# Kernel optimization log

Measured on AMD Instinct MI355X. Metric: run time of the kernel, lower is better.

The kernel has to match this reference:

```python
import jax, jax.numpy as jnp
import numpy as np

N = 50000      # ncount
L = 4          # number of wavelet scales
E = 1600000    # nnz per sparse wavelet matrix
C_IN = 128
C_OUT = 128


def setup_inputs() -> dict:
    key = jax.random.key(0)
    ks = jax.random.split(key, 7)
    return {
        "phi_indices": jax.random.randint(ks[0], (L, 2, E), 0, N, dtype=jnp.int32),
        "phi_values": jax.random.uniform(ks[1], (L, E), dtype=jnp.float32),
        "phi_inverse_indices": jax.random.randint(ks[2], (L, 2, E), 0, N, dtype=jnp.int32),
        "phi_inverse_values": jax.random.uniform(ks[3], (L, E), dtype=jnp.float32),
        "features": jax.random.normal(ks[4], (N, L, C_IN), dtype=jnp.float32),
        "weight_matrix": jax.random.normal(ks[5], (C_IN, C_OUT), dtype=jnp.float32) * (6.0 / (C_IN + C_OUT)) ** 0.5,
        "diagonal_weight_filter": jax.random.uniform(ks[6], (N,), dtype=jnp.float32, minval=0.9, maxval=1.1),
    }


def _spmm(idx, vals, X):
    # sparse [N,N] (COO rows=idx[0], cols=idx[1]) @ dense X [N,C]
    row, col = idx[0], idx[1]
    return jax.ops.segment_sum(vals[:, None] * X[col], row, num_segments=N)


def reference(phi_indices, phi_values, phi_inverse_indices, phi_inverse_values,
              features, weight_matrix, diagonal_weight_filter):
    # Original: (phi_i @ diag(theta) @ phi_inv_i) @ (features[:,i,:] @ W)
    # Applied right-to-left via associativity -> three streaming spmm-style ops,
    # never materializing the N x N product matrix.
    def per_scale(p_idx, p_val, pi_idx, pi_val, feat_i):
        y = feat_i @ weight_matrix                 # [N, C_OUT]
        y = _spmm(pi_idx, pi_val, y)               # phi_inverse @ y
        y = y * diagonal_weight_filter[:, None]    # diag(theta) @ y
        return _spmm(p_idx, p_val, y)              # phi @ y

    feats_lf = jnp.moveaxis(features, 1, 0)        # [L, N, C_IN]
    out = jax.vmap(per_scale)(phi_indices, phi_values,
                              phi_inverse_indices, phi_inverse_values, feats_lf)
    return jnp.moveaxis(out, 0, 1)                 # [N, L, C_OUT]
```

## Files before the change

kernel.cpp:

```cpp
#include <hip/hip_runtime.h>

#define N_NODES 50000
#define L_SCALES 4
#define E_NNZ 1600000
#define C 128
#define NL (N_NODES * L_SCALES)

#define ELL_W 64
#define OVF_CAP 8192

#define RPB 16
#define NB (N_NODES / RPB)
#define NSUB 8
#define SCAP 112
#define GROUP 4
#define BT_STRIDE 16

__global__ __launch_bounds__(256) void gemm_all(
    const float* __restrict__ feat,
    const float* __restrict__ W,
    float* __restrict__ Y)
{
    __shared__ float4 Xs4[64 * 32];

    int t = threadIdx.x;
    int l = t & 63;
    int c0 = __builtin_amdgcn_readfirstlane((t >> 6) << 5);
    size_t r0 = (size_t)blockIdx.x * 64;

    const float4* feat4 = (const float4*)(feat + r0 * C);
    for (int i = t; i < 64 * 32; i += 256) {
        int row = i >> 5, slot = i & 31;
        Xs4[(row << 5) | (slot ^ (row & 31))] = feat4[i];
    }
    __syncthreads();

    float acc[32];
    #pragma unroll
    for (int j = 0; j < 32; ++j) acc[j] = 0.f;

    int m = l & 31;
    for (int kt = 0; kt < C; kt += 8) {
        float4 xa = Xs4[(l << 5) | ((kt >> 2) ^ m)];
        float4 xb = Xs4[(l << 5) | (((kt >> 2) + 1) ^ m)];
        float x8[8];
        x8[0] = xa.x; x8[1] = xa.y; x8[2] = xa.z; x8[3] = xa.w;
        x8[4] = xb.x; x8[5] = xb.y; x8[6] = xb.z; x8[7] = xb.w;
        #pragma unroll
        for (int kk = 0; kk < 8; ++kk) {
            const float* wr = W + (size_t)(kt + kk) * C + c0;
            #pragma unroll
            for (int j = 0; j < 32; ++j)
                acc[j] = fmaf(x8[kk], wr[j], acc[j]);
        }
    }

    float* orow = Y + (r0 + l) * C + c0;
    #pragma unroll
    for (int j4 = 0; j4 < 8; ++j4)
        ((float4*)orow)[j4] = make_float4(acc[4*j4], acc[4*j4+1], acc[4*j4+2], acc[4*j4+3]);
}

__global__ __launch_bounds__(256) void partition_edges(
    const int*   __restrict__ rows,
    const int*   __restrict__ cols,
    const float* __restrict__ vals,
    uint2* __restrict__ bkt,
    int*   __restrict__ btail,
    int* __restrict__ ovf_n, int* __restrict__ ovf_row,
    int* __restrict__ ovf_col, float* __restrict__ ovf_val)
{
    int e = blockIdx.x * 256 + threadIdx.x;
    if (e >= E_NNZ) return;
    int s = blockIdx.x & (NSUB - 1);
    int r = rows[e];
    int c = cols[e];
    float v = vals[e];
    int b = r >> 4;
    int pos = atomicAdd(&btail[(s * NB + b) * BT_STRIDE], 1);
    if (pos < SCAP) {
        bkt[((size_t)s * NB + b) * SCAP + pos] =
            make_uint2((unsigned)c | ((unsigned)(r & (RPB - 1)) << 16), __float_as_uint(v));
    } else {
        int k = atomicAdd(ovf_n, 1);
        if (k < OVF_CAP) { ovf_row[k] = r; ovf_col[k] = c; ovf_val[k] = v; }
    }
}

__global__ __launch_bounds__(256) void ell_from_buckets(
    const uint2* __restrict__ bkt,
    const int*   __restrict__ btail,
    uint2* __restrict__ ell,
    int*   __restrict__ cnt,
    int* __restrict__ ovf_n, int* __restrict__ ovf_row,
    int* __restrict__ ovf_col, float* __restrict__ ovf_val)
{
    __shared__ __align__(16) uint2 ell_s[GROUP * RPB][ELL_W];
    __shared__ int lcnt[GROUP * RPB];

    int t  = threadIdx.x;
    int b0 = blockIdx.x * GROUP;
    int r0 = b0 * RPB;

    if (t < GROUP * RPB) lcnt[t] = 0;
    __syncthreads();

    for (int g = 0; g < GROUP; ++g) {
        int b = b0 + g;
        if (b >= NB) break;
        for (int s = 0; s < NSUB; ++s) {
            int n = btail[(s * NB + b) * BT_STRIDE];
            if (n > SCAP) n = SCAP;
            for (int i = t; i < n; i += 256) {
                uint2 rec = bkt[((size_t)s * NB + b) * SCAP + i];
                int lr = g * RPB + (int)(rec.x >> 16);
                int pos = atomicAdd(&lcnt[lr], 1);
                if (pos < ELL_W) {
                    ell_s[lr][pos] = make_uint2(rec.x & 0xFFFFu, rec.y);
                } else {
                    int k = atomicAdd(ovf_n, 1);
                    if (k < OVF_CAP) {
                        ovf_row[k] = r0 + lr;
                        ovf_col[k] = (int)(rec.x & 0xFFFFu);
                        ovf_val[k] = __uint_as_float(rec.y);
                    }
                }
            }
        }
    }
    __syncthreads();

    const uint4* src = (const uint4*)&ell_s[0][0];
    for (int i = t; i < GROUP * RPB * (ELL_W / 2); i += 256) {
        int row = r0 + (i >> 5);
        if (row < N_NODES)
            ((uint4*)ell)[(size_t)row * (ELL_W / 2) + (i & 31)] = src[i];
    }
    if (t < GROUP * RPB) {
        int row = r0 + t;
        if (row < N_NODES) cnt[row] = lcnt[t];
    }
}

__global__ __launch_bounds__(256) void spmm_ell(
    const uint2* __restrict__ ell,
    const int*   __restrict__ cnt,
    const int*   __restrict__ ovf_n,
    const int*   __restrict__ ovf_row,
    const int*   __restrict__ ovf_col,
    const float* __restrict__ ovf_val,
    const float* __restrict__ X,
    const float* __restrict__ row_scale,
    float*       __restrict__ out,
    int x_stride, int out_stride)
{
    int row  = (blockIdx.x * 256 + threadIdx.x) >> 6;
    int lane = threadIdx.x & 63;

    int n   = cnt[row];
    int ncl = n < ELL_W ? n : ELL_W;

    uint2 rec = make_uint2(0u, 0u);
    if (lane < ncl) rec = ell[(size_t)row * ELL_W + lane];
    int mycol = (int)rec.x;
    int myval = (int)rec.y;

    float2 acc = {0.f, 0.f};
    int j = 0;
    for (; j + 8 <= ncl; j += 8) {
        float2 x[8];
        #pragma unroll
        for (int u = 0; u < 8; ++u) {
            int c = __builtin_amdgcn_readlane(mycol, j + u);
            x[u] = ((const float2*)(X + (size_t)c * x_stride))[lane];
        }
        #pragma unroll
        for (int u = 0; u < 8; ++u) {
            float v = __uint_as_float((unsigned)__builtin_amdgcn_readlane(myval, j + u));
            acc.x = fmaf(v, x[u].x, acc.x);
            acc.y = fmaf(v, x[u].y, acc.y);
        }
    }
    for (; j < ncl; ++j) {
        int   c = __builtin_amdgcn_readlane(mycol, j);
        float v = __uint_as_float((unsigned)__builtin_amdgcn_readlane(myval, j));
        float2 x = ((const float2*)(X + (size_t)c * x_stride))[lane];
        acc.x = fmaf(v, x.x, acc.x);
        acc.y = fmaf(v, x.y, acc.y);
    }

    int m = *ovf_n;
    if (m > 0) {
        if (m > OVF_CAP) m = OVF_CAP;
        for (int k = 0; k < m; ++k) {
            if (ovf_row[k] == row) {
                float v = ovf_val[k];
                float2 x = ((const float2*)(X + (size_t)ovf_col[k] * x_stride))[lane];
                acc.x = fmaf(v, x.x, acc.x);
                acc.y = fmaf(v, x.y, acc.y);
            }
        }
    }

    if (row_scale) {
        float s = row_scale[row];
        acc.x *= s;
        acc.y *= s;
    }
    ((float2*)(out + (size_t)row * out_stride))[lane] = acc;
}

extern "C" void kernel_launch(void* const* d_in, const int* in_sizes, int n_in,
                              void* d_out, int out_size, void* d_ws, size_t ws_size,
                              hipStream_t stream) {
    const int*   phi_idx  = (const int*)  d_in[0];
    const float* phi_val  = (const float*)d_in[1];
    const int*   pinv_idx = (const int*)  d_in[2];
    const float* pinv_val = (const float*)d_in[3];
    const float* feat     = (const float*)d_in[4];
    const float* W        = (const float*)d_in[5];
    const float* theta    = (const float*)d_in[6];
    float* out = (float*)d_out;

    float* Z       = (float*)d_ws;
    uint2* bkt     = (uint2*)(Z + (size_t)N_NODES * C);
    uint2* ell     = bkt + (size_t)NSUB * NB * SCAP;
    int*   cnt     = (int*)(ell + (size_t)N_NODES * ELL_W);
    int*   btail   = cnt + N_NODES;
    int*   ovf_n   = btail + NSUB * NB * BT_STRIDE;
    int*   ovf_row = ovf_n + 1;
    int*   ovf_col = ovf_row + OVF_CAP;
    float* ovf_val = (float*)(ovf_col + OVF_CAP);

    dim3 blk(256);
    int gemmGrid = NL / 64;
    int partGrid = (E_NNZ + 255) / 256;
    int ellGrid  = (NB + GROUP - 1) / GROUP;
    int spmmGrid = N_NODES * 64 / 256;

    gemm_all<<<gemmGrid, blk, 0, stream>>>(feat, W, out);

    for (int l = 0; l < L_SCALES; ++l) {
        hipMemsetAsync(btail, 0, (NSUB * NB * BT_STRIDE + 1) * sizeof(int), stream);
        partition_edges<<<partGrid, blk, 0, stream>>>(
            pinv_idx + (size_t)l * 2 * E_NNZ,
            pinv_idx + (size_t)l * 2 * E_NNZ + E_NNZ,
            pinv_val + (size_t)l * E_NNZ,
            bkt, btail, ovf_n, ovf_row, ovf_col, ovf_val);
        ell_from_buckets<<<ellGrid, blk, 0, stream>>>(
            bkt, btail, ell, cnt, ovf_n, ovf_row, ovf_col, ovf_val);
        spmm_ell<<<spmmGrid, blk, 0, stream>>>(
            ell, cnt, ovf_n, ovf_row, ovf_col, ovf_val,
            out + (size_t)l * C, theta, Z, L_SCALES * C, C);

        hipMemsetAsync(btail, 0, (NSUB * NB * BT_STRIDE + 1) * sizeof(int), stream);
        partition_edges<<<partGrid, blk, 0, stream>>>(
            phi_idx + (size_t)l * 2 * E_NNZ,
            phi_idx + (size_t)l * 2 * E_NNZ + E_NNZ,
            phi_val + (size_t)l * E_NNZ,
            bkt, btail, ovf_n, ovf_row, ovf_col, ovf_val);
        ell_from_buckets<<<ellGrid, blk, 0, stream>>>(
            bkt, btail, ell, cnt, ovf_n, ovf_row, ovf_col, ovf_val);
        spmm_ell<<<spmmGrid, blk, 0, stream>>>(
            ell, cnt, ovf_n, ovf_row, ovf_col, ovf_val,
            Z, nullptr, out + (size_t)l * C, C, L_SCALES * C);
    }
}
```

Baseline: 1.862 ms.

## Retile dense GEMM with shared W tiles and order SpMM gathers by column segment

The feature-times-weight GEMM now uses a 128x128 block tile. A and W are both staged through shared memory in k-chunks of 16, and each thread computes an 8x8 outer product instead of reading W from global memory per row. The SpMM row kernel replaces its 8-way unrolled gather loop with a loop over 13 column segments. Each segment uses a ballot to visit that row's nonzeros in segment order, so concurrent waves tend to touch similar regions of X and cache locality should improve. The catch is that gathers are now serialized one at a time with no unrolled memory-level parallelism, and the loop always runs all 13 ballots.

Result: no change. 1.872 ms (+0.5%).

```diff
diff --git a/kernel.cpp b/kernel.cpp
--- a/kernel.cpp
+++ b/kernel.cpp
@@ -16,49 +16,71 @@
 #define GROUP 4
 #define BT_STRIDE 16
 
+#define SEG_SHIFT 12
+#define NSEG 13
+
 __global__ __launch_bounds__(256) void gemm_all(
     const float* __restrict__ feat,
     const float* __restrict__ W,
     float* __restrict__ Y)
 {
-    __shared__ float4 Xs4[64 * 32];
-
-    int t = threadIdx.x;
-    int l = t & 63;
-    int c0 = __builtin_amdgcn_readfirstlane((t >> 6) << 5);
-    size_t r0 = (size_t)blockIdx.x * 64;
-
-    const float4* feat4 = (const float4*)(feat + r0 * C);
-    for (int i = t; i < 64 * 32; i += 256) {
-        int row = i >> 5, slot = i & 31;
-        Xs4[(row << 5) | (slot ^ (row & 31))] = feat4[i];
-    }
-    __syncthreads();
-
-    float acc[32];
+    __shared__ float As[16][132];
+    __shared__ float Ws[16][128];
+
+    int t  = threadIdx.x;
+    int ty = t >> 4;
+    int tx = t & 15;
+    size_t r0 = (size_t)blockIdx.x * 128;
+
+    float acc[8][8];
     #pragma unroll
-    for (int j = 0; j < 32; ++j) acc[j] = 0.f;
-
-    int m = l & 31;
-    for (int kt = 0; kt < C; kt += 8) {
-        float4 xa = Xs4[(l << 5) | ((kt >> 2) ^ m)];
-        float4 xb = Xs4[(l << 5) | (((kt >> 2) + 1) ^ m)];
-        float x8[8];
-        x8[0] = xa.x; x8[1] = xa.y; x8[2] = xa.z; x8[3] = xa.w;
-        x8[4] = xb.x; x8[5] = xb.y; x8[6] = xb.z; x8[7] = xb.w;
+    for (int i = 0; i < 8; ++i)
         #pragma unroll
-        for (int kk = 0; kk < 8; ++kk) {
-            const float* wr = W + (size_t)(kt + kk) * C + c0;
+        for (int j = 0; j < 8; ++j) acc[i][j] = 0.f;
+
+    for (int kt = 0; kt < C; kt += 16) {
+        __syncthreads();
+        #pragma unroll
+        for (int jj = 0; jj < 2; ++jj) {
+            int q = t + 256 * jj;
+            int row = q >> 2, pc = q & 3;
+            size_t r = r0 + row;
+            float4 f = (r < (size_t)NL) ? ((const float4*)(feat + r * C + kt))[pc]
+                                        : make_float4(0.f, 0.f, 0.f, 0.f);
+            As[pc * 4 + 0][row] = f.x;
+            As[pc * 4 + 1][row] = f.y;
+            As[pc * 4 + 2][row] = f.z;
+            As[pc * 4 + 3][row] = f.w;
+            int kr = q >> 5, wpc = q & 31;
+            ((float4*)&Ws[kr][0])[wpc] = ((const float4*)(W + (size_t)(kt + kr) * C))[wpc];
+        }
+        __syncthreads();
+
+        #pragma unroll
+        for (int kk = 0; kk < 16; ++kk) {
+            float4 a0 = *(const float4*)&As[kk][ty * 8];
+            float4 a1 = *(const float4*)&As[kk][ty * 8 + 4];
+            float4 w0 = *(const float4*)&Ws[kk][tx * 4];
+            float4 w1 = *(const float4*)&Ws[kk][64 + tx * 4];
+            float a[8] = {a0.x, a0.y, a0.z, a0.w, a1.x, a1.y, a1.z, a1.w};
+            float w[8] = {w0.x, w0.y, w0.z, w0.w, w1.x, w1.y, w1.z, w1.w};
             #pragma unroll
-            for (int j = 0; j < 32; ++j)
-                acc[j] = fmaf(x8[kk], wr[j], acc[j]);
-        }
-    }
-
-    float* orow = Y + (r0 + l) * C + c0;
+            for (int i = 0; i < 8; ++i)
+                #pragma unroll
+                for (int j = 0; j < 8; ++j)
+                    acc[i][j] = fmaf(a[i], w[j], acc[i][j]);
+        }
+    }
+
     #pragma unroll
-    for (int j4 = 0; j4 < 8; ++j4)
-        ((float4*)orow)[j4] = make_float4(acc[4*j4], acc[4*j4+1], acc[4*j4+2], acc[4*j4+3]);
+    for (int i = 0; i < 8; ++i) {
+        size_t r = r0 + ty * 8 + i;
+        if (r < (size_t)NL) {
+            float* orow = Y + r * C;
+            *(float4*)(orow + tx * 4)      = make_float4(acc[i][0], acc[i][1], acc[i][2], acc[i][3]);
+            *(float4*)(orow + 64 + tx * 4) = make_float4(acc[i][4], acc[i][5], acc[i][6], acc[i][7]);
+        }
+    }
 }
 
 __global__ __launch_bounds__(256) void partition_edges(
@@ -164,29 +186,20 @@
     if (lane < ncl) rec = ell[(size_t)row * ELL_W + lane];
     int mycol = (int)rec.x;
     int myval = (int)rec.y;
+    int myseg = (lane < ncl) ? (mycol >> SEG_SHIFT) : 64;
 
     float2 acc = {0.f, 0.f};
-    int j = 0;
-    for (; j + 8 <= ncl; j += 8) {
-        float2 x[8];
-        #pragma unroll
-        for (int u = 0; u < 8; ++u) {
-            int c = __builtin_amdgcn_readlane(mycol, j + u);
-            x[u] = ((const float2*)(X + (size_t)c * x_stride))[lane];
-        }
-        #pragma unroll
-        for (int u = 0; u < 8; ++u) {
-            float v = __uint_as_float((unsigned)__builtin_amdgcn_readlane(myval, j + u));
-            acc.x = fmaf(v, x[u].x, acc.x);
-            acc.y = fmaf(v, x[u].y, acc.y);
-        }
-    }
-    for (; j < ncl; ++j) {
-        int   c = __builtin_amdgcn_readlane(mycol, j);
-        float v = __uint_as_float((unsigned)__builtin_amdgcn_readlane(myval, j));
-        float2 x = ((const float2*)(X + (size_t)c * x_stride))[lane];
-        acc.x = fmaf(v, x.x, acc.x);
-        acc.y = fmaf(v, x.y, acc.y);
+    for (int s = 0; s < NSEG; ++s) {
+        unsigned long long mask = __ballot(myseg == s);
+        while (mask) {
+            int j = __builtin_ctzll(mask);
+            mask &= mask - 1;
+            int   c = __builtin_amdgcn_readlane(mycol, j);
+            float v = __uint_as_float((unsigned)__builtin_amdgcn_readlane(myval, j));
+            float2 x = ((const float2*)(X + (size_t)c * x_stride))[lane];
+            acc.x = fmaf(v, x.x, acc.x);
+            acc.y = fmaf(v, x.y, acc.y);
+        }
     }
 
     int m = *ovf_n;
@@ -233,7 +246,7 @@
     float* ovf_val = (float*)(ovf_col + OVF_CAP);
 
     dim3 blk(256);
-    int gemmGrid = NL / 64;
+    int gemmGrid = (NL + 127) / 128;
     int partGrid = (E_NNZ + 255) / 256;
     int ellGrid  = (NB + GROUP - 1) / GROUP;
     int spmmGrid = N_NODES * 64 / 256;
```
